# Optimization experiments

Measured on AMD Instinct MI355X. Metric: run time of the kernel, lower is better.

The kernel has to match this reference:

```python
import jax, jax.numpy as jnp
import numpy as np

B, T, C, H = 512, 256, 768, 64
NEG = -1e9  # finite stand-in for -inf; exp(NEG - max) underflows to exactly 0 in fp32


def setup_inputs() -> dict:
    key = jax.random.key(0)
    kx, kq, kk, kv, kp = jax.random.split(key, 5)
    # xavier_uniform bound for a (H, C) torch Linear weight: sqrt(6/(C+H))
    bound = float(np.sqrt(6.0 / (C + H)))
    return {
        "x": jax.random.normal(kx, (B, T, C), dtype=jnp.float32),
        "Wq": jax.random.uniform(kq, (C, H), jnp.float32, -bound, bound),
        "Wk": jax.random.uniform(kk, (C, H), jnp.float32, -bound, bound),
        "Wv": jax.random.uniform(kv, (C, H), jnp.float32, -bound, bound),
        "pad_mask": jax.random.randint(kp, (B, T), 0, 2, dtype=jnp.int32),
    }


def reference(x, Wq, Wk, Wv, pad_mask):
    # Projections (torch Linear without bias: x @ W.T; W stored here pre-transposed as [C,H])
    q = x @ Wq  # [B,T,H]
    k = x @ Wk
    v = x @ Wv
    scores = jnp.einsum("bth,bsh->bts", q, k) / (H ** 0.5)  # [B,T,T]
    causal = jnp.tril(jnp.ones((T, T), dtype=bool))
    # pad_mask.unsqueeze(-1)==0 masks entire query rows i where pad_mask[b,i]==0
    mask = causal[None, :, :] & (pad_mask[:, :, None] != 0)  # [B,T,T]
    weights = jax.nn.softmax(jnp.where(mask, scores, NEG), axis=-1)
    # torch: fully -inf rows -> softmax NaN -> replaced with zeros
    row_valid = mask.any(axis=-1)  # [B,T]
    weights = jnp.where(row_valid[:, :, None], weights, 0.0)
    # dropout is identity in eval mode
    return weights @ v  # [B,T,H]
```

## Files before the change

### kernel.cpp

```cpp
#include <hip/hip_runtime.h>
#include <hip/hip_bf16.h>

typedef unsigned short u16;
typedef unsigned int u32;
typedef __attribute__((ext_vector_type(8))) short short8;
typedef __attribute__((ext_vector_type(4))) float f32x4;
typedef __attribute__((ext_vector_type(4))) u16 u16x4;

static constexpr int Bb = 512, Tt = 256, Cc = 768, Hh = 64;

__device__ __forceinline__ u16 f2bf(float f) {
    __hip_bfloat16 h = __float2bfloat16(f);
    union { __hip_bfloat16 h; u16 u; } v; v.h = h;
    return v.u;
}

__device__ __forceinline__ void gll16(const u16* g, u16* l) {
    __builtin_amdgcn_global_load_lds(
        (const __attribute__((address_space(1))) u32*)g,
        (__attribute__((address_space(3))) u32*)l, 16, 0, 0);
}

__global__ void wt_kernel(const float* __restrict__ Wq, const float* __restrict__ Wk,
                          const float* __restrict__ Wv, u16* __restrict__ Wf) {
    int idx = blockIdx.x * 256 + threadIdx.x;
    int n = idx / Cc, k = idx % Cc;
    const float* W = (n < 64) ? Wq : (n < 128) ? Wk : Wv;
    float val = W[k * Hh + (n & 63)];
    int nt = n >> 4, fr = n & 15;
    int kc = k >> 6, ksub = (k >> 5) & 1, fk = k & 31;
    Wf[kc * 12288 + (ksub * 12 + nt) * 512 + (fr + ((fk >> 3) << 4)) * 8 + (fk & 7)] = f2bf(val);
}

__global__ __launch_bounds__(512, 2) void fused_kernel(
        const float* __restrict__ x, const u16* __restrict__ Wf,
        const int* __restrict__ pad, float* __restrict__ out) {
    __shared__ u16 smem[59392];
    char* smB = (char*)smem;

    const int tid = threadIdx.x;
    const int w = tid >> 6, l = tid & 63;
    const int lrow = l & 15, lgrp = l >> 4;
    const int b = blockIdx.x;
    const int cswz = (lrow & 7) << 4;
    const int tt0 = w, tt1 = 15 - w;

    const float* xg = x + ((size_t)b * Tt + (tid >> 4)) * Cc + (tid & 15) * 4;

    float4 xr[8];
    f32x4 acc[2][12];
#pragma unroll
    for (int i = 0; i < 2; ++i)
#pragma unroll
        for (int j = 0; j < 12; ++j) acc[i][j] = (f32x4)0.f;

#define XLOAD(kc_)                                                             \
    _Pragma("unroll")                                                          \
    for (int j = 0; j < 8; ++j)                                                \
        xr[j] = *(const float4*)(xg + (size_t)j * 32 * Cc + (kc_) * 64);

#define XWRITE(nb_)                                                            \
    {                                                                          \
        char* xb_ = smB + (nb_) * 32768;                                       \
        _Pragma("unroll")                                                      \
        for (int j = 0; j < 8; ++j) {                                          \
            int row = j * 32 + (tid >> 4);                                     \
            u16x4 pk;                                                          \
            pk[0] = f2bf(xr[j].x); pk[1] = f2bf(xr[j].y);                      \
            pk[2] = f2bf(xr[j].z); pk[3] = f2bf(xr[j].w);                      \
            *(u16x4*)(xb_ + ((row * 128 + (tid & 15) * 8) ^ ((row & 7) << 4))) = pk; \
        }                                                                      \
    }

#define WSTAGE(kc_, nb_)                                                       \
    {                                                                          \
        u16* wl_ = smem + 32768 + (nb_) * 12288;                               \
        const u16* wg_ = Wf + (size_t)(kc_) * 12288;                           \
        _Pragma("unroll")                                                      \
        for (int p = 0; p < 3; ++p)                                            \
            gll16(wg_ + (p * 8 + w) * 512 + l * 8, wl_ + (p * 8 + w) * 512);   \
    }

#define COMPUTE(cur_)                                                          \
    {                                                                          \
        const char* xb = smB + (cur_) * 32768;                                 \
        const char* wb = smB + 65536 + (cur_) * 24576;                         \
        _Pragma("unroll")                                                      \
        for (int ksub = 0; ksub < 2; ++ksub) {                                 \
            short8 bfr[12], af[2];                                             \
            _Pragma("unroll")                                                  \
            for (int nt = 0; nt < 12; ++nt)                                    \
                bfr[nt] = *(const short8*)(wb + (ksub * 12 + nt) * 1024 + l * 16); \
            af[0] = *(const short8*)(xb +                                      \
                (((tt0 * 16 + lrow) * 128 + ksub * 64 + lgrp * 16) ^ cswz));   \
            af[1] = *(const short8*)(xb +                                      \
                (((tt1 * 16 + lrow) * 128 + ksub * 64 + lgrp * 16) ^ cswz));   \
            _Pragma("unroll")                                                  \
            for (int mrep = 0; mrep < 2; ++mrep)                               \
                _Pragma("unroll")                                              \
                for (int nt = 0; nt < 12; ++nt)                                \
                    acc[mrep][nt] = __builtin_amdgcn_mfma_f32_16x16x32_bf16(   \
                        af[mrep], bfr[nt], acc[mrep][nt], 0, 0, 0);            \
        }                                                                      \
    }

    XLOAD(0); WSTAGE(0, 0); XWRITE(0);
    __syncthreads();
    for (int kc = 0; kc < 12; ++kc) {
        const int cur = kc & 1;
        if (kc < 11) { WSTAGE(kc + 1, cur ^ 1); XLOAD(kc + 1); }
        COMPUTE(cur);
        if (kc < 11) { XWRITE(cur ^ 1); }
        __syncthreads();
    }
#undef XLOAD
#undef XWRITE
#undef WSTAGE
#undef COMPUTE

#pragma unroll
    for (int mrep = 0; mrep < 2; ++mrep) {
        const int tt = (mrep == 0) ? tt0 : tt1;
        const int s0 = tt * 16;
#pragma unroll
        for (int nt = 0; nt < 12; ++nt) {
            f32x4 a = acc[mrep][nt];
            if (nt < 4) {
                int h = nt * 16 + lrow;
#pragma unroll
                for (int r = 0; r < 4; ++r) {
                    int row = s0 + lgrp * 4 + r;
                    *(u16*)(smB + 65536 + ((row * 128 + h * 2) ^ ((row & 7) << 4))) = f2bf(a[r]);
                }
            } else if (nt < 8) {
                int h = (nt - 4) * 16 + lrow;
#pragma unroll
                for (int r = 0; r < 4; ++r) {
                    int s = s0 + lgrp * 4 + r;
                    *(u16*)(smB + ((s * 128 + h * 2) ^ ((s & 7) << 4))) = f2bf(a[r]);
                }
            } else {
                int h = (nt - 8) * 16 + lrow;
                int s = s0 + lgrp * 4;
                u16x4 pk;
                pk[0] = f2bf(a[0]); pk[1] = f2bf(a[1]);
                pk[2] = f2bf(a[2]); pk[3] = f2bf(a[3]);
                *(u16x4*)(smB + 32768 + h * 512 + ((s * 2) ^ ((h & 15) << 4))) = pk;
            }
        }
    }
    __syncthreads();

    short8 qfr[2][2];
#pragma unroll
    for (int mt = 0; mt < 2; ++mt) {
        const int tt = (mt == 0) ? tt0 : tt1;
#pragma unroll
        for (int kk = 0; kk < 2; ++kk)
            qfr[mt][kk] = *(const short8*)(smB + 65536 +
                (((tt * 16 + lrow) * 128 + kk * 64 + lgrp * 16) ^ cswz));
    }

    char* pbase = smB + 98304 + w * 2560;
#pragma unroll
    for (int mt = 0; mt < 2; ++mt) {
        const int tt = (mt == 0) ? tt0 : tt1;
        const int i0 = tt * 16;

        f32x4 sreg[16];
#pragma unroll
        for (int t = 0; t < 16; ++t) {
            if (t <= tt) {
                short8 k0 = *(const short8*)(smB +
                    (((t * 16 + lrow) * 128 + lgrp * 16) ^ cswz));
                short8 k1 = *(const short8*)(smB +
                    (((t * 16 + lrow) * 128 + 64 + lgrp * 16) ^ cswz));
                f32x4 s = (f32x4)0.f;
                s = __builtin_amdgcn_mfma_f32_16x16x32_bf16(qfr[mt][0], k0, s, 0, 0, 0);
                s = __builtin_amdgcn_mfma_f32_16x16x32_bf16(qfr[mt][1], k1, s, 0, 0, 0);
                if (t == tt) {
#pragma unroll
                    for (int r = 0; r < 4; ++r) {
                        int i = i0 + lgrp * 4 + r;
                        int sidx = t * 16 + lrow;
                        sreg[t][r] = (sidx <= i) ? s[r] * 0.125f : -1e30f;
                    }
                } else {
#pragma unroll
                    for (int r = 0; r < 4; ++r) sreg[t][r] = s[r] * 0.125f;
                }
            }
        }

        f32x4 mx = (f32x4)(-1e30f);
#pragma unroll
        for (int t = 0; t < 16; ++t)
            if (t <= tt)
#pragma unroll
                for (int r = 0; r < 4; ++r) mx[r] = fmaxf(mx[r], sreg[t][r]);
#pragma unroll
        for (int m = 1; m <= 8; m <<= 1)
#pragma unroll
            for (int r = 0; r < 4; ++r) mx[r] = fmaxf(mx[r], __shfl_xor(mx[r], m, 64));

        f32x4 sm = (f32x4)0.f;
#pragma unroll
        for (int t = 0; t < 16; ++t)
            if (t <= tt)
#pragma unroll
                for (int r = 0; r < 4; ++r) {
                    float p = __expf(sreg[t][r] - mx[r]);
                    sreg[t][r] = p;
                    sm[r] += p;
                }
#pragma unroll
        for (int m = 1; m <= 8; m <<= 1)
#pragma unroll
            for (int r = 0; r < 4; ++r) sm[r] += __shfl_xor(sm[r], m, 64);

        float inv[4];
#pragma unroll
        for (int r = 0; r < 4; ++r) {
            int i = i0 + lgrp * 4 + r;
            inv[r] = (pad[b * Tt + i] != 0) ? (1.0f / sm[r]) : 0.0f;
        }

        f32x4 o[4];
#pragma unroll
        for (int ht = 0; ht < 4; ++ht) o[ht] = (f32x4)0.f;
#pragma unroll
        for (int ks = 0; ks < 8; ++ks) {
            if (2 * ks <= tt) {
                char* pb = pbase + (ks & 1) * 1280;
#pragma unroll
                for (int r = 0; r < 4; ++r) {
                    int prow = lgrp * 4 + r;
                    *(u16*)(pb + prow * 80 + lrow * 2) = f2bf(sreg[2 * ks][r]);
                    u16 pv2 = (2 * ks + 1 <= tt) ? f2bf(sreg[2 * ks + 1][r]) : (u16)0;
                    *(u16*)(pb + prow * 80 + 32 + lrow * 2) = pv2;
                }
                short8 pa = *(const short8*)(pb + lrow * 80 + lgrp * 16);
#pragma unroll
                for (int ht = 0; ht < 4; ++ht) {
                    short8 vfr = *(const short8*)(smB + 32768 + (ht * 16 + lrow) * 512 +
                        ((ks * 64 + lgrp * 16) ^ (lrow << 4)));
                    o[ht] = __builtin_amdgcn_mfma_f32_16x16x32_bf16(pa, vfr, o[ht], 0, 0, 0);
                }
            }
        }

        float* outp = out + ((size_t)b * Tt + i0) * Hh;
#pragma unroll
        for (int r = 0; r < 4; ++r)
#pragma unroll
            for (int ht = 0; ht < 4; ++ht)
                outp[(lgrp * 4 + r) * Hh + ht * 16 + lrow] = o[ht][r] * inv[r];
    }
}

extern "C" void kernel_launch(void* const* d_in, const int* in_sizes, int n_in,
                              void* d_out, int out_size, void* d_ws, size_t ws_size,
                              hipStream_t stream) {
    const float* x  = (const float*)d_in[0];
    const float* Wq = (const float*)d_in[1];
    const float* Wk = (const float*)d_in[2];
    const float* Wv = (const float*)d_in[3];
    const int* pad  = (const int*)d_in[4];
    float* out = (float*)d_out;

    u16* Wf = (u16*)d_ws;

    wt_kernel<<<576, 256, 0, stream>>>(Wq, Wk, Wv, Wf);
    fused_kernel<<<Bb, 512, 0, stream>>>(x, Wf, pad, out);
}
```

Baseline: 120.2 us.

## Single-buffer projection GEMM with 128-wide K chunks and register-prefetched x

The projection GEMM drops the double-buffered 64-wide K chunks and uses single LDS buffers holding 128-wide K chunks, so six iterations replace twelve. The next chunk of x is prefetched into two register sets around the compute, and the weight layout is changed to a row-swizzled form matching the new tile. LDS use falls slightly and the P buffer is moved to reuse the weight region, which needs an extra barrier. In exchange, global-to-LDS staging no longer overlaps compute and there are two barriers per iteration.

Result: slower. 154.9 us (+28.9%).

```diff
diff --git a/kernel.cpp b/kernel.cpp
--- a/kernel.cpp
+++ b/kernel.cpp
@@ -27,15 +27,15 @@
     int n = idx / Cc, k = idx % Cc;
     const float* W = (n < 64) ? Wq : (n < 128) ? Wk : Wv;
     float val = W[k * Hh + (n & 63)];
-    int nt = n >> 4, fr = n & 15;
-    int kc = k >> 6, ksub = (k >> 5) & 1, fk = k & 31;
-    Wf[kc * 12288 + (ksub * 12 + nt) * 512 + (fr + ((fk >> 3) << 4)) * 8 + (fk & 7)] = f2bf(val);
+    int kc = k >> 7, kl = k & 127;
+    int lb = (n * 256 + kl * 2) ^ ((n & 7) << 4);
+    Wf[kc * 24576 + (lb >> 1)] = f2bf(val);
 }
 
 __global__ __launch_bounds__(512, 2) void fused_kernel(
         const float* __restrict__ x, const u16* __restrict__ Wf,
         const int* __restrict__ pad, float* __restrict__ out) {
-    __shared__ u16 smem[59392];
+    __shared__ u16 smem[57344];
     char* smB = (char*)smem;
 
     const int tid = threadIdx.x;
@@ -45,76 +45,78 @@
     const int cswz = (lrow & 7) << 4;
     const int tt0 = w, tt1 = 15 - w;
 
-    const float* xg = x + ((size_t)b * Tt + (tid >> 4)) * Cc + (tid & 15) * 4;
-
-    float4 xr[8];
+    const int xrow0 = tid >> 5, xcol = tid & 31;
+    const int cxw = (xrow0 & 7) << 4;
+    const float* xg = x + ((size_t)b * Tt + xrow0) * Cc + xcol * 4;
+
+    float4 xrA[8], xrB[8];
     f32x4 acc[2][12];
 #pragma unroll
     for (int i = 0; i < 2; ++i)
 #pragma unroll
         for (int j = 0; j < 12; ++j) acc[i][j] = (f32x4)0.f;
 
-#define XLOAD(kc_)                                                             \
+#define XLOADH(kc_, R_, h_)                                                    \
     _Pragma("unroll")                                                          \
-    for (int j = 0; j < 8; ++j)                                                \
-        xr[j] = *(const float4*)(xg + (size_t)j * 32 * Cc + (kc_) * 64);
-
-#define XWRITE(nb_)                                                            \
+    for (int j2 = 0; j2 < 8; ++j2)                                             \
+        R_[j2] = *(const float4*)(xg + (size_t)((h_) * 8 + j2) * 16 * Cc + (kc_) * 128);
+
+#define XWRITEH(R_, h_)                                                        \
+    _Pragma("unroll")                                                          \
+    for (int j2 = 0; j2 < 8; ++j2) {                                           \
+        int row = xrow0 + 16 * ((h_) * 8 + j2);                                \
+        u16x4 pk;                                                              \
+        pk[0] = f2bf(R_[j2].x); pk[1] = f2bf(R_[j2].y);                        \
+        pk[2] = f2bf(R_[j2].z); pk[3] = f2bf(R_[j2].w);                        \
+        *(u16x4*)(smB + row * 256 + ((xcol * 8) ^ cxw)) = pk;                  \
+    }
+
+#define WSTAGE(kc_)                                                            \
     {                                                                          \
-        char* xb_ = smB + (nb_) * 32768;                                       \
+        const u16* wg_ = Wf + (size_t)(kc_) * 24576;                           \
         _Pragma("unroll")                                                      \
-        for (int j = 0; j < 8; ++j) {                                          \
-            int row = j * 32 + (tid >> 4);                                     \
-            u16x4 pk;                                                          \
-            pk[0] = f2bf(xr[j].x); pk[1] = f2bf(xr[j].y);                      \
-            pk[2] = f2bf(xr[j].z); pk[3] = f2bf(xr[j].w);                      \
-            *(u16x4*)(xb_ + ((row * 128 + (tid & 15) * 8) ^ ((row & 7) << 4))) = pk; \
-        }                                                                      \
-    }
-
-#define WSTAGE(kc_, nb_)                                                       \
-    {                                                                          \
-        u16* wl_ = smem + 32768 + (nb_) * 12288;                               \
-        const u16* wg_ = Wf + (size_t)(kc_) * 12288;                           \
+        for (int p = 0; p < 6; ++p)                                            \
+            gll16(wg_ + p * 4096 + tid * 8, smem + 32768 + p * 4096 + tid * 8);\
+    }
+
+#define COMPUTE()                                                              \
+    _Pragma("unroll")                                                          \
+    for (int ksub = 0; ksub < 4; ++ksub) {                                     \
+        short8 bfr[12], af[2];                                                 \
         _Pragma("unroll")                                                      \
-        for (int p = 0; p < 3; ++p)                                            \
-            gll16(wg_ + (p * 8 + w) * 512 + l * 8, wl_ + (p * 8 + w) * 512);   \
-    }
-
-#define COMPUTE(cur_)                                                          \
-    {                                                                          \
-        const char* xb = smB + (cur_) * 32768;                                 \
-        const char* wb = smB + 65536 + (cur_) * 24576;                         \
+        for (int nt = 0; nt < 12; ++nt)                                        \
+            bfr[nt] = *(const short8*)(smB + 65536 +                           \
+                (((nt * 16 + lrow) * 256 + ksub * 64 + lgrp * 16) ^ cswz));    \
+        af[0] = *(const short8*)(smB +                                         \
+            (((tt0 * 16 + lrow) * 256 + ksub * 64 + lgrp * 16) ^ cswz));       \
+        af[1] = *(const short8*)(smB +                                         \
+            (((tt1 * 16 + lrow) * 256 + ksub * 64 + lgrp * 16) ^ cswz));       \
         _Pragma("unroll")                                                      \
-        for (int ksub = 0; ksub < 2; ++ksub) {                                 \
-            short8 bfr[12], af[2];                                             \
+        for (int mrep = 0; mrep < 2; ++mrep)                                   \
             _Pragma("unroll")                                                  \
             for (int nt = 0; nt < 12; ++nt)                                    \
-                bfr[nt] = *(const short8*)(wb + (ksub * 12 + nt) * 1024 + l * 16); \
-            af[0] = *(const short8*)(xb +                                      \
-                (((tt0 * 16 + lrow) * 128 + ksub * 64 + lgrp * 16) ^ cswz));   \
-            af[1] = *(const short8*)(xb +                                      \
-                (((tt1 * 16 + lrow) * 128 + ksub * 64 + lgrp * 16) ^ cswz));   \
-            _Pragma("unroll")                                                  \
-            for (int mrep = 0; mrep < 2; ++mrep)                               \
-                _Pragma("unroll")                                              \
-                for (int nt = 0; nt < 12; ++nt)                                \
-                    acc[mrep][nt] = __builtin_amdgcn_mfma_f32_16x16x32_bf16(   \
-                        af[mrep], bfr[nt], acc[mrep][nt], 0, 0, 0);            \
-        }                                                                      \
-    }
-
-    XLOAD(0); WSTAGE(0, 0); XWRITE(0);
+                acc[mrep][nt] = __builtin_amdgcn_mfma_f32_16x16x32_bf16(       \
+                    af[mrep], bfr[nt], acc[mrep][nt], 0, 0, 0);                \
+    }
+
+    XLOADH(0, xrA, 0); XLOADH(0, xrB, 1);
+    XWRITEH(xrA, 0); XWRITEH(xrB, 1);
+    WSTAGE(0);
     __syncthreads();
-    for (int kc = 0; kc < 12; ++kc) {
-        const int cur = kc & 1;
-        if (kc < 11) { WSTAGE(kc + 1, cur ^ 1); XLOAD(kc + 1); }
-        COMPUTE(cur);
-        if (kc < 11) { XWRITE(cur ^ 1); }
+
+    for (int kc = 0; kc < 6; ++kc) {
+        if (kc < 5) { XLOADH(kc + 1, xrA, 0); }
+        COMPUTE();
+        if (kc < 5) { XLOADH(kc + 1, xrB, 1); }
         __syncthreads();
-    }
-#undef XLOAD
-#undef XWRITE
+        if (kc < 5) {
+            XWRITEH(xrA, 0); XWRITEH(xrB, 1);
+            WSTAGE(kc + 1);
+            __syncthreads();
+        }
+    }
+#undef XLOADH
+#undef XWRITEH
 #undef WSTAGE
 #undef COMPUTE
 
@@ -160,8 +162,9 @@
             qfr[mt][kk] = *(const short8*)(smB + 65536 +
                 (((tt * 16 + lrow) * 128 + kk * 64 + lgrp * 16) ^ cswz));
     }
-
-    char* pbase = smB + 98304 + w * 2560;
+    __syncthreads();
+
+    char* pbase = smB + 65536 + w * 2560;
 #pragma unroll
     for (int mt = 0; mt < 2; ++mt) {
         const int tt = (mt == 0) ? tt0 : tt1;
```

## Prefetch x two chunks ahead via register double-buffer and stage W through registers

Applied to the files above, without the earlier changes.

The projection main loop now keeps two register sets of x so the global load for chunk k+2 is issued while chunk k is computed. The direct global-to-LDS load of W is replaced by a register load followed by an LDS store. Barriers become a custom lgkmcnt-only wait, so outstanding global loads no longer stall at each barrier. LDS shrinks because the P buffer now reuses the Q region behind an extra barrier. The extra register arrays raise VGPR pressure under the 512x2 launch bound and may cause spills.

New measurement: 126.5 us. 1.05x slower.

```diff
diff --git a/kernel.cpp b/kernel.cpp
--- a/kernel.cpp
+++ b/kernel.cpp
@@ -13,12 +13,6 @@
     __hip_bfloat16 h = __float2bfloat16(f);
     union { __hip_bfloat16 h; u16 u; } v; v.h = h;
     return v.u;
-}
-
-__device__ __forceinline__ void gll16(const u16* g, u16* l) {
-    __builtin_amdgcn_global_load_lds(
-        (const __attribute__((address_space(1))) u32*)g,
-        (__attribute__((address_space(3))) u32*)l, 16, 0, 0);
 }
 
 __global__ void wt_kernel(const float* __restrict__ Wq, const float* __restrict__ Wk,
@@ -35,7 +29,7 @@
 __global__ __launch_bounds__(512, 2) void fused_kernel(
         const float* __restrict__ x, const u16* __restrict__ Wf,
         const int* __restrict__ pad, float* __restrict__ out) {
-    __shared__ u16 smem[59392];
+    __shared__ u16 smem[57344];
     char* smB = (char*)smem;
 
     const int tid = threadIdx.x;
@@ -47,38 +41,43 @@
 
     const float* xg = x + ((size_t)b * Tt + (tid >> 4)) * Cc + (tid & 15) * 4;
 
-    float4 xr[8];
+    float4 xrA[8], xrB[8];
+    short8 wr[3];
     f32x4 acc[2][12];
 #pragma unroll
     for (int i = 0; i < 2; ++i)
 #pragma unroll
         for (int j = 0; j < 12; ++j) acc[i][j] = (f32x4)0.f;
 
-#define XLOAD(kc_)                                                             \
+#define XLOAD(kc_, R_)                                                         \
     _Pragma("unroll")                                                          \
     for (int j = 0; j < 8; ++j)                                                \
-        xr[j] = *(const float4*)(xg + (size_t)j * 32 * Cc + (kc_) * 64);
-
-#define XWRITE(nb_)                                                            \
+        R_[j] = *(const float4*)(xg + (size_t)j * 32 * Cc + (kc_) * 64);
+
+#define XWRITE(R_, nb_)                                                        \
     {                                                                          \
         char* xb_ = smB + (nb_) * 32768;                                       \
         _Pragma("unroll")                                                      \
         for (int j = 0; j < 8; ++j) {                                          \
             int row = j * 32 + (tid >> 4);                                     \
             u16x4 pk;                                                          \
-            pk[0] = f2bf(xr[j].x); pk[1] = f2bf(xr[j].y);                      \
-            pk[2] = f2bf(xr[j].z); pk[3] = f2bf(xr[j].w);                      \
+            pk[0] = f2bf(R_[j].x); pk[1] = f2bf(R_[j].y);                      \
+            pk[2] = f2bf(R_[j].z); pk[3] = f2bf(R_[j].w);                      \
             *(u16x4*)(xb_ + ((row * 128 + (tid & 15) * 8) ^ ((row & 7) << 4))) = pk; \
         }                                                                      \
     }
 
-#define WSTAGE(kc_, nb_)                                                       \
+#define WLOADR(kc_)                                                            \
+    _Pragma("unroll")                                                          \
+    for (int p = 0; p < 3; ++p)                                                \
+        wr[p] = *(const short8*)(Wf + (size_t)(kc_) * 12288 + (p * 8 + w) * 512 + l * 8);
+
+#define WWRITE(nb_)                                                            \
     {                                                                          \
         u16* wl_ = smem + 32768 + (nb_) * 12288;                               \
-        const u16* wg_ = Wf + (size_t)(kc_) * 12288;                           \
         _Pragma("unroll")                                                      \
         for (int p = 0; p < 3; ++p)                                            \
-            gll16(wg_ + (p * 8 + w) * 512 + l * 8, wl_ + (p * 8 + w) * 512);   \
+            *(short8*)(wl_ + (p * 8 + w) * 512 + l * 8) = wr[p];               \
     }
 
 #define COMPUTE(cur_)                                                          \
@@ -104,19 +103,49 @@
         }                                                                      \
     }
 
-    XLOAD(0); WSTAGE(0, 0); XWRITE(0);
+#define LBAR() asm volatile("s_waitcnt lgkmcnt(0)\n\ts_barrier" ::: "memory")
+
+    XLOAD(0, xrA);
+    WLOADR(0);
+    XLOAD(1, xrB);
+    XWRITE(xrA, 0);
+    WWRITE(0);
+    LBAR();
+
+#pragma unroll 1
+    for (int ii = 0; ii < 5; ++ii) {
+        const int ke = ii * 2;
+        {
+            WLOADR(ke + 1);
+            XLOAD(ke + 2, xrA);
+            COMPUTE(0);
+            XWRITE(xrB, 1);
+            WWRITE(1);
+            LBAR();
+        }
+        {
+            WLOADR(ke + 2);
+            XLOAD(ke + 3, xrB);
+            COMPUTE(1);
+            XWRITE(xrA, 0);
+            WWRITE(0);
+            LBAR();
+        }
+    }
+
+    WLOADR(11);
+    COMPUTE(0);
+    XWRITE(xrB, 1);
+    WWRITE(1);
+    LBAR();
+    COMPUTE(1);
     __syncthreads();
-    for (int kc = 0; kc < 12; ++kc) {
-        const int cur = kc & 1;
-        if (kc < 11) { WSTAGE(kc + 1, cur ^ 1); XLOAD(kc + 1); }
-        COMPUTE(cur);
-        if (kc < 11) { XWRITE(cur ^ 1); }
-        __syncthreads();
-    }
 #undef XLOAD
 #undef XWRITE
-#undef WSTAGE
+#undef WLOADR
+#undef WWRITE
 #undef COMPUTE
+#undef LBAR
 
 #pragma unroll
     for (int mrep = 0; mrep < 2; ++mrep) {
@@ -160,8 +189,9 @@
             qfr[mt][kk] = *(const short8*)(smB + 65536 +
                 (((tt * 16 + lrow) * 128 + kk * 64 + lgrp * 16) ^ cswz));
     }
-
-    char* pbase = smB + 98304 + w * 2560;
+    __syncthreads();
+
+    char* pbase = smB + 65536 + w * 2560;
 #pragma unroll
     for (int mt = 0; mt < 2; ++mt) {
         const int tt = (mt == 0) ? tt0 : tt1;
```
